# Optimization experiments

Hardware: AMD Instinct MI355X
Metric: run time of the kernel (lower is better)

## Reference

```python
import jax, jax.numpy as jnp
import numpy as np

# Static pyramid shapes (H, W) per level; must match setup_inputs().
SPATIAL_SHAPES = [(128, 128), (64, 64), (32, 32), (16, 16)]
N, LQ, D_MODEL, M, L, P = 2, 21760, 256, 8, 4, 4
D_HEAD = D_MODEL // M
LEN_IN = sum(h * w for h, w in SPATIAL_SHAPES)


def _bilinear_sample(v, grid, H, W):
    """torch.grid_sample(mode=bilinear, padding=zeros, align_corners=False).
    v: [B, H, W, D], grid: [B, Q, P, 2] (x, y) in [-1, 1] -> [B, Q, P, D]."""
    gx = (grid[..., 0] + 1.0) * (W * 0.5) - 0.5
    gy = (grid[..., 1] + 1.0) * (H * 0.5) - 0.5
    x0 = jnp.floor(gx)
    y0 = jnp.floor(gy)
    wx1 = gx - x0
    wy1 = gy - y0
    b = jnp.arange(v.shape[0])[:, None, None]

    def gather(yi, xi):
        valid = (xi >= 0) & (xi <= W - 1) & (yi >= 0) & (yi <= H - 1)
        xc = jnp.clip(xi, 0, W - 1).astype(jnp.int32)
        yc = jnp.clip(yi, 0, H - 1).astype(jnp.int32)
        return v[b, yc, xc] * valid[..., None].astype(v.dtype)

    return (gather(y0, x0) * ((1 - wy1) * (1 - wx1))[..., None]
            + gather(y0, x0 + 1) * ((1 - wy1) * wx1)[..., None]
            + gather(y0 + 1, x0) * (wy1 * (1 - wx1))[..., None]
            + gather(y0 + 1, x0 + 1) * (wy1 * wx1)[..., None])


def setup_inputs() -> dict:
    key = jax.random.key(0)
    ks = jax.random.split(key, 12)
    s = 0.02
    return {
        "query": jax.random.normal(ks[0], (N, LQ, D_MODEL), jnp.float32),
        "reference_points": jax.random.uniform(ks[1], (N, LQ, L, 2), jnp.float32),
        "value": jax.random.normal(ks[2], (N, LEN_IN, D_MODEL), jnp.float32),
        "value_spatial_shapes": jnp.array(SPATIAL_SHAPES, jnp.int32),
        "W_val": jax.random.normal(ks[3], (D_MODEL, D_MODEL), jnp.float32) * s,
        "b_val": jnp.zeros((D_MODEL,), jnp.float32),
        "W_off": jax.random.normal(ks[4], (D_MODEL, M * L * P * 2), jnp.float32) * s,
        "b_off": jax.random.normal(ks[5], (M * L * P * 2,), jnp.float32) * s,
        "W_attn": jax.random.normal(ks[6], (D_MODEL, M * L * P), jnp.float32) * s,
        "b_attn": jnp.zeros((M * L * P,), jnp.float32),
        "W_out": jax.random.normal(ks[7], (D_MODEL, D_MODEL), jnp.float32) * s,
        "b_out": jnp.zeros((D_MODEL,), jnp.float32),
    }


def reference(query, reference_points, value, value_spatial_shapes,
              W_val, b_val, W_off, b_off, W_attn, b_attn, W_out, b_out):
    # value_spatial_shapes is treated as static (SPATIAL_SHAPES) for jit safety.
    v = (value @ W_val + b_val).reshape(N, LEN_IN, M, D_HEAD)
    off = (query @ W_off + b_off).reshape(N, LQ, M, L, P, 2)
    aw = jax.nn.softmax((query @ W_attn + b_attn).reshape(N, LQ, M, L * P), axis=-1)
    aw = aw.reshape(N, LQ, M, L, P)
    # normalizer stacks (W, H) -> x normalized by W, y by H
    norm = jnp.array([[w, h] for h, w in SPATIAL_SHAPES], dtype=query.dtype)
    loc = reference_points[:, :, None, :, None, :] + off / norm[None, None, None, :, None, :]
    grid = 2.0 * loc - 1.0  # [N, LQ, M, L, P, 2]

    out = jnp.zeros((N * M, LQ, D_HEAD), query.dtype)
    start = 0
    for lid, (H, W) in enumerate(SPATIAL_SHAPES):
        vl = v[:, start:start + H * W].reshape(N, H, W, M, D_HEAD)
        vl = vl.transpose(0, 3, 1, 2, 4).reshape(N * M, H, W, D_HEAD)
        gl = grid[:, :, :, lid].transpose(0, 2, 1, 3, 4).reshape(N * M, LQ, P, 2)
        sl = _bilinear_sample(vl, gl, H, W)  # [N*M, LQ, P, D]
        wl = aw[:, :, :, lid].transpose(0, 2, 1, 3).reshape(N * M, LQ, P)
        out = out + jnp.einsum('bqpd,bqp->bqd', sl, wl)
        start += H * W

    out = out.reshape(N, M, LQ, D_HEAD).transpose(0, 2, 1, 3).reshape(N, LQ, D_MODEL)
    return out @ W_out + b_out
```

## Files before the change

### kernel.cpp

```cpp
#include <hip/hip_runtime.h>

typedef __attribute__((ext_vector_type(8))) short short8;
typedef __attribute__((ext_vector_type(4))) float floatx4;

#define N_    2
#define LQ_   21760
#define D_    256
#define M_    8
#define L_    4
#define P_    4
#define DH_   32
#define LEN_  21760
#define BQ    16

__constant__ int c_start[4] = {0, 16384, 20480, 21504};
__constant__ int c_HW[4]    = {128, 64, 32, 16};

#define WT_BYTE_OFF 22282240u

__device__ __forceinline__ unsigned short f2bf(float f) {
  unsigned int u = __builtin_bit_cast(unsigned int, f);
  u += 0x7fffu + ((u >> 16) & 1u);
  return (unsigned short)(u >> 16);
}
__device__ __forceinline__ float bf2f(unsigned short s) {
  return __builtin_bit_cast(float, ((unsigned int)s) << 16);
}
__device__ __forceinline__ float bflo(unsigned int u) {
  return __builtin_bit_cast(float, u << 16);
}
__device__ __forceinline__ float bfhi(unsigned int u) {
  return __builtin_bit_cast(float, u & 0xffff0000u);
}

__global__ __launch_bounds__(256) void prep_kernel(
    const float* __restrict__ Woff, const float* __restrict__ Watt,
    const float* __restrict__ Wout, const float* __restrict__ Wv,
    unsigned short* __restrict__ wt) {
  const int b = blockIdx.x, t = threadIdx.x;
  const float* src; int ncols, n; unsigned short* dst;
  if (b < 256)      { src = Woff; ncols = 256; n = b;       dst = wt + 0      + n * 256; }
  else if (b < 384) { src = Watt; ncols = 128; n = b - 256; dst = wt + 65536  + n * 256; }
  else if (b < 640) { src = Wout; ncols = 256; n = b - 384; dst = wt + 98304  + n * 256; }
  else              { src = Wv;   ncols = 256; n = b - 640; dst = wt + 163840 + n * 256; }
  dst[t] = f2bf(src[(size_t)t * ncols + n]);
}

__global__ __launch_bounds__(256, 2) void vproj_kernel(
    const float* __restrict__ value, const unsigned short* __restrict__ Wvt,
    const float* __restrict__ bv, unsigned short* __restrict__ vout) {
  __shared__ unsigned short vs[64][264];
  const int t = threadIdx.x;
  const int r0 = blockIdx.x * 64;
  {
    const int c2 = (t & 127) * 2;
    const int rb = t >> 7;
#pragma unroll
    for (int i = 0; i < 32; ++i) {
      int rr = rb + i * 2;
      float2 v = *(const float2*)(value + (size_t)(r0 + rr) * D_ + c2);
      *(unsigned int*)&vs[rr][c2] = (unsigned int)f2bf(v.x) | ((unsigned int)f2bf(v.y) << 16);
    }
  }
  __syncthreads();
  const int wave = t >> 6, lane = t & 63;
  const int arow = wave * 16 + (lane & 15);
  const int kg = (lane >> 4) * 8;
  floatx4 acc[16] = {};
  for (int kk = 0; kk < 8; ++kk) {
    const int k0 = kk * 32;
    short8 af = *(const short8*)&vs[arow][k0 + kg];
#pragma unroll
    for (int ct = 0; ct < 16; ++ct) {
      const int col = ct * 16 + (lane & 15);
      short8 bf = *(const short8*)(Wvt + col * 256 + k0 + kg);
      acc[ct] = __builtin_amdgcn_mfma_f32_16x16x32_bf16(af, bf, acc[ct], 0, 0, 0);
    }
  }
  const int n = (r0 >= LEN_) ? 1 : 0;
  const int pixbase = r0 - n * LEN_ + wave * 16 + ((lane >> 4) * 4);
#pragma unroll
  for (int ct = 0; ct < 16; ++ct) {
    const int gc = ct * 16 + (lane & 15);
    const int m = gc >> 5, d = gc & 31;
    const float bb = bv[gc];
    unsigned short* ob = vout + ((size_t)(n * M_ + m) * LEN_) * DH_ + d;
#pragma unroll
    for (int j = 0; j < 4; ++j)
      ob[(size_t)(pixbase + j) * DH_] = f2bf(acc[ct][j] + bb);
  }
}

__global__ __launch_bounds__(256, 5) void msda_kernel(
    const float* __restrict__ query, const float* __restrict__ refp,
    const unsigned short* __restrict__ wt,
    const float* __restrict__ boff, const float* __restrict__ batt,
    const float* __restrict__ bout,
    const unsigned short* __restrict__ vproj, float* __restrict__ out) {
  __shared__ unsigned short qs[BQ][264];
  __shared__ unsigned short offb[BQ][256];
  __shared__ float awb[BQ][128];
  __shared__ short idxs2[2][128];
  __shared__ float wls2[2][128][4];

  const int t = threadIdx.x;
  const int lb = (blockIdx.x & 7) * 340 + (blockIdx.x >> 3);
  const int qg0 = lb * BQ;
  const int n = qg0 / LQ_;

  {
    const int c2 = (t & 127) * 2;
    const int rb = t >> 7;
#pragma unroll
    for (int i = 0; i < 8; ++i) {
      int rr = rb + i * 2;
      float2 v = *(const float2*)(query + (size_t)(qg0 + rr) * D_ + c2);
      *(unsigned int*)&qs[rr][c2] = (unsigned int)f2bf(v.x) | ((unsigned int)f2bf(v.y) << 16);
    }
  }
  __syncthreads();

  const int wave = t >> 6, lane = t & 63;
  const int arow = lane & 15;
  const int kg = (lane >> 4) * 8;
  const int row0 = (lane >> 4) * 4;

  {
    floatx4 acc[6] = {};
    for (int kk = 0; kk < 8; ++kk) {
      const int k0 = kk * 32;
      short8 af = *(const short8*)&qs[arow][k0 + kg];
#pragma unroll
      for (int i = 0; i < 6; ++i) {
        const int col = wave * 96 + i * 16 + (lane & 15);
        const unsigned short* bp = (col < 256) ? (wt + col * 256)
                                               : (wt + 65536 + (col - 256) * 256);
        short8 bf = *(const short8*)(bp + k0 + kg);
        acc[i] = __builtin_amdgcn_mfma_f32_16x16x32_bf16(af, bf, acc[i], 0, 0, 0);
      }
    }
#pragma unroll
    for (int i = 0; i < 6; ++i) {
      const int col = wave * 96 + i * 16 + (lane & 15);
      if (col < 256) {
        const float bb = boff[col];
#pragma unroll
        for (int j = 0; j < 4; ++j) offb[row0 + j][col] = f2bf(acc[i][j] + bb);
      } else {
        const float bb = batt[col - 256];
#pragma unroll
        for (int j = 0; j < 4; ++j) awb[row0 + j][col - 256] = acc[i][j] + bb;
      }
    }
  }
  __syncthreads();

  if (t < 128) {
    const int q = t >> 3, m = t & 7;
    float v[16]; float mx = -1e30f;
#pragma unroll
    for (int s = 0; s < 16; ++s) { v[s] = awb[q][m * 16 + s]; mx = fmaxf(mx, v[s]); }
    float sum = 0.f;
#pragma unroll
    for (int s = 0; s < 16; ++s) { v[s] = __expf(v[s] - mx); sum += v[s]; }
    const float inv = 1.f / sum;
#pragma unroll
    for (int s = 0; s < 16; ++s) awb[q][m * 16 + s] = v[s] * inv;
  }
  __syncthreads();

  const int m_g = t >> 5;
  const int g = t & 31;
  const int sp   = g >> 4;
  const int rsel = (g >> 3) & 1;
  const int csel = (g >> 2) & 1;
  const int wsel = (g >> 2) & 3;
  const int doct = g & 3;
  const char* vbyte = (const char*)vproj + (size_t)(n * M_ + m_g) * LEN_ * DH_ * 2;

  for (int q = 0; q < BQ; ++q) {
    const int slot = q & 1;
    if (t < 128) {
      const int l = (t >> 2) & 3;
      const int Wl = c_HW[l];
      const int st = c_start[l];
      const float rx = refp[(((size_t)(qg0 + q)) * L_ + l) * 2 + 0];
      const float ry = refp[(((size_t)(qg0 + q)) * L_ + l) * 2 + 1];
      const float gx = rx * (float)Wl + bf2f(offb[q][2 * t])     - 0.5f;
      const float gy = ry * (float)Wl + bf2f(offb[q][2 * t + 1]) - 0.5f;
      const float fx0 = floorf(gx), fy0 = floorf(gy);
      const int x0 = (int)fx0, y0 = (int)fy0;
      const float wx1 = gx - fx0, wy1 = gy - fy0;
      const float wx0 = 1.f - wx1, wy0 = 1.f - wy1;
      const float a = awb[q][t];
      const bool vx0 = (x0 >= 0) && (x0 < Wl);
      const bool vx1 = (x0 + 1 >= 0) && (x0 + 1 < Wl);
      const bool vy0 = (y0 >= 0) && (y0 < Wl);
      const bool vy1 = (y0 + 1 >= 0) && (y0 + 1 < Wl);
      idxs2[slot][t] = (short)(st + y0 * Wl + x0);
      wls2[slot][t][0] = (vy0 && vx0) ? wy0 * wx0 * a : 0.f;
      wls2[slot][t][1] = (vy0 && vx1) ? wy0 * wx1 * a : 0.f;
      wls2[slot][t][2] = (vy1 && vx0) ? wy1 * wx0 * a : 0.f;
      wls2[slot][t][3] = (vy1 && vx1) ? wy1 * wx1 * a : 0.f;
    }
    __syncthreads();

    const int sidb = m_g * 16;
    uint4 u0, u1, u2, u3, u4, u5, u6, u7;
    float w0, w1, w2, w3, w4, w5, w6, w7;
#define GLD(i, WLC)                                                        \
    {                                                                      \
      const int s_ = 2 * (i) + sp;                                         \
      const int ix_ = (int)idxs2[slot][sidb + s_];                         \
      w##i = wls2[slot][sidb + s_][wsel];                                  \
      int ofs_ = (ix_ + rsel * (WLC) + csel) * 64 + doct * 16;             \
      ofs_ = (ofs_ > 0) ? ofs_ : 0;                                        \
      u##i = *(const uint4*)(vbyte + ofs_);                                \
    }
    GLD(0, 128) GLD(1, 128) GLD(2, 64) GLD(3, 64)
    GLD(4, 32)  GLD(5, 32)  GLD(6, 16) GLD(7, 16)
#undef GLD

    float acc0 = 0.f, acc1 = 0.f, acc2 = 0.f, acc3 = 0.f;
    float acc4 = 0.f, acc5 = 0.f, acc6 = 0.f, acc7 = 0.f;
#define FMA8(i)                                                            \
    acc0 += bflo(u##i.x) * w##i; acc1 += bfhi(u##i.x) * w##i;              \
    acc2 += bflo(u##i.y) * w##i; acc3 += bfhi(u##i.y) * w##i;              \
    acc4 += bflo(u##i.z) * w##i; acc5 += bfhi(u##i.z) * w##i;              \
    acc6 += bflo(u##i.w) * w##i; acc7 += bfhi(u##i.w) * w##i;
    FMA8(0) FMA8(1) FMA8(2) FMA8(3) FMA8(4) FMA8(5) FMA8(6) FMA8(7)
#undef FMA8

    acc0 += __shfl_xor(acc0, 4);  acc1 += __shfl_xor(acc1, 4);
    acc2 += __shfl_xor(acc2, 4);  acc3 += __shfl_xor(acc3, 4);
    acc4 += __shfl_xor(acc4, 4);  acc5 += __shfl_xor(acc5, 4);
    acc6 += __shfl_xor(acc6, 4);  acc7 += __shfl_xor(acc7, 4);
    acc0 += __shfl_xor(acc0, 8);  acc1 += __shfl_xor(acc1, 8);
    acc2 += __shfl_xor(acc2, 8);  acc3 += __shfl_xor(acc3, 8);
    acc4 += __shfl_xor(acc4, 8);  acc5 += __shfl_xor(acc5, 8);
    acc6 += __shfl_xor(acc6, 8);  acc7 += __shfl_xor(acc7, 8);
    acc0 += __shfl_xor(acc0, 16); acc1 += __shfl_xor(acc1, 16);
    acc2 += __shfl_xor(acc2, 16); acc3 += __shfl_xor(acc3, 16);
    acc4 += __shfl_xor(acc4, 16); acc5 += __shfl_xor(acc5, 16);
    acc6 += __shfl_xor(acc6, 16); acc7 += __shfl_xor(acc7, 16);

    if (g < 4) {
      uint4 st4;
      st4.x = (unsigned int)f2bf(acc0) | ((unsigned int)f2bf(acc1) << 16);
      st4.y = (unsigned int)f2bf(acc2) | ((unsigned int)f2bf(acc3) << 16);
      st4.z = (unsigned int)f2bf(acc4) | ((unsigned int)f2bf(acc5) << 16);
      st4.w = (unsigned int)f2bf(acc6) | ((unsigned int)f2bf(acc7) << 16);
      *(uint4*)&qs[q][m_g * 32 + doct * 8] = st4;
    }
  }
  __syncthreads();

  {
    floatx4 acc[4] = {};
    for (int kk = 0; kk < 8; ++kk) {
      const int k0 = kk * 32;
      short8 af = *(const short8*)&qs[arow][k0 + kg];
#pragma unroll
      for (int i = 0; i < 4; ++i) {
        const int col = wave * 64 + i * 16 + (lane & 15);
        short8 bf = *(const short8*)(wt + 98304 + col * 256 + k0 + kg);
        acc[i] = __builtin_amdgcn_mfma_f32_16x16x32_bf16(af, bf, acc[i], 0, 0, 0);
      }
    }
#pragma unroll
    for (int i = 0; i < 4; ++i) {
      const int col = wave * 64 + i * 16 + (lane & 15);
      const float bb = bout[col];
#pragma unroll
      for (int j = 0; j < 4; ++j)
        out[(size_t)(qg0 + row0 + j) * D_ + col] = acc[i][j] + bb;
    }
  }
}

extern "C" void kernel_launch(void* const* d_in, const int* in_sizes, int n_in,
                              void* d_out, int out_size, void* d_ws, size_t ws_size,
                              hipStream_t stream) {
  const float* query = (const float*)d_in[0];
  const float* refp  = (const float*)d_in[1];
  const float* value = (const float*)d_in[2];
  const float* Wv    = (const float*)d_in[4];
  const float* bv    = (const float*)d_in[5];
  const float* Woff  = (const float*)d_in[6];
  const float* boff  = (const float*)d_in[7];
  const float* Watt  = (const float*)d_in[8];
  const float* batt  = (const float*)d_in[9];
  const float* Wout  = (const float*)d_in[10];
  const float* bout  = (const float*)d_in[11];
  float* out = (float*)d_out;

  unsigned short* vproj = (unsigned short*)d_ws;
  unsigned short* wt    = (unsigned short*)((char*)d_ws + WT_BYTE_OFF);
  const unsigned short* Wvt = wt + 163840;

  dim3 blk(256);
  hipLaunchKernelGGL(prep_kernel, dim3(896), blk, 0, stream, Woff, Watt, Wout, Wv, wt);
  hipLaunchKernelGGL(vproj_kernel, dim3((N_ * LEN_) / 64), blk, 0, stream, value, Wvt, bv, vproj);
  hipLaunchKernelGGL(msda_kernel, dim3((N_ * LQ_) / BQ), blk, 0, stream,
                     query, refp, wt, boff, batt, bout, vproj, out);
}
```

Baseline: 239.6 us.

## Make sampling stage wave-local, removing per-query block barriers

Each wave now computes its own sampling indices and bilinear weights, for its two heads and two queries at a time, into wave-private shared slots. This removes the per-query __syncthreads and the 128-thread-only setup phase. Reference points are preloaded into registers up front, and a waves_per_eu hint is added. The risk is higher register pressure from the rp array and the unrolled two-query body. Correctness also depends on wave-level lockstep for the shared-memory handoff, since there is no explicit barrier.

```diff
diff --git a/kernel.cpp b/kernel.cpp
--- a/kernel.cpp
+++ b/kernel.cpp
@@ -91,7 +91,9 @@
   }
 }
 
-__global__ __launch_bounds__(256, 5) void msda_kernel(
+__global__ __launch_bounds__(256, 5)
+__attribute__((amdgpu_waves_per_eu(4, 5)))
+void msda_kernel(
     const float* __restrict__ query, const float* __restrict__ refp,
     const unsigned short* __restrict__ wt,
     const float* __restrict__ boff, const float* __restrict__ batt,
@@ -100,8 +102,8 @@
   __shared__ unsigned short qs[BQ][264];
   __shared__ unsigned short offb[BQ][256];
   __shared__ float awb[BQ][128];
-  __shared__ short idxs2[2][128];
-  __shared__ float wls2[2][128][4];
+  __shared__ short sidx[4][2][2][16];
+  __shared__ float swls[4][2][2][16][4];
 
   const int t = threadIdx.x;
   const int lb = (blockIdx.x & 7) * 340 + (blockIdx.x >> 3);
@@ -169,88 +171,96 @@
   }
   __syncthreads();
 
-  const int m_g = t >> 5;
-  const int g = t & 31;
-  const int sp   = g >> 4;
-  const int rsel = (g >> 3) & 1;
-  const int csel = (g >> 2) & 1;
-  const int wsel = (g >> 2) & 3;
-  const int doct = g & 3;
+  const int qo  = lane >> 5;
+  const int sh  = (lane >> 4) & 1;
+  const int ss  = lane & 15;
+  const int slv = ss >> 2;
+  const int WlS = 128 >> slv;
+  const int stS = c_start[slv];
+  const int st_eq = (2 * wave + sh) * 16 + ss;
+  const int hg = lane >> 5;
+  const int m_g = 2 * wave + hg;
+  const int g = lane & 31;
+  const int sp = g >> 4, rsel = (g >> 3) & 1, csel = (g >> 2) & 1;
+  const int wsel = (g >> 2) & 3, doct = g & 3;
   const char* vbyte = (const char*)vproj + (size_t)(n * M_ + m_g) * LEN_ * DH_ * 2;
 
-  for (int q = 0; q < BQ; ++q) {
-    const int slot = q & 1;
-    if (t < 128) {
-      const int l = (t >> 2) & 3;
-      const int Wl = c_HW[l];
-      const int st = c_start[l];
-      const float rx = refp[(((size_t)(qg0 + q)) * L_ + l) * 2 + 0];
-      const float ry = refp[(((size_t)(qg0 + q)) * L_ + l) * 2 + 1];
-      const float gx = rx * (float)Wl + bf2f(offb[q][2 * t])     - 0.5f;
-      const float gy = ry * (float)Wl + bf2f(offb[q][2 * t + 1]) - 0.5f;
+  const float2* refp2 = (const float2*)refp;
+  float2 rp[8];
+#pragma unroll
+  for (int e = 0; e < 8; ++e)
+    rp[e] = refp2[(size_t)(qg0 + 2 * e + qo) * 4 + slv];
+
+  for (int e = 0; e < 8; ++e) {
+    {
+      const int q = 2 * e + qo;
+      const float gx = rp[e].x * (float)WlS + bf2f(offb[q][2 * st_eq])     - 0.5f;
+      const float gy = rp[e].y * (float)WlS + bf2f(offb[q][2 * st_eq + 1]) - 0.5f;
       const float fx0 = floorf(gx), fy0 = floorf(gy);
       const int x0 = (int)fx0, y0 = (int)fy0;
       const float wx1 = gx - fx0, wy1 = gy - fy0;
       const float wx0 = 1.f - wx1, wy0 = 1.f - wy1;
-      const float a = awb[q][t];
-      const bool vx0 = (x0 >= 0) && (x0 < Wl);
-      const bool vx1 = (x0 + 1 >= 0) && (x0 + 1 < Wl);
-      const bool vy0 = (y0 >= 0) && (y0 < Wl);
-      const bool vy1 = (y0 + 1 >= 0) && (y0 + 1 < Wl);
-      idxs2[slot][t] = (short)(st + y0 * Wl + x0);
-      wls2[slot][t][0] = (vy0 && vx0) ? wy0 * wx0 * a : 0.f;
-      wls2[slot][t][1] = (vy0 && vx1) ? wy0 * wx1 * a : 0.f;
-      wls2[slot][t][2] = (vy1 && vx0) ? wy1 * wx0 * a : 0.f;
-      wls2[slot][t][3] = (vy1 && vx1) ? wy1 * wx1 * a : 0.f;
-    }
-    __syncthreads();
-
-    const int sidb = m_g * 16;
-    uint4 u0, u1, u2, u3, u4, u5, u6, u7;
-    float w0, w1, w2, w3, w4, w5, w6, w7;
+      const float a = awb[q][st_eq];
+      const bool vx0 = (x0 >= 0) && (x0 < WlS);
+      const bool vx1 = (x0 + 1 >= 0) && (x0 + 1 < WlS);
+      const bool vy0 = (y0 >= 0) && (y0 < WlS);
+      const bool vy1 = (y0 + 1 >= 0) && (y0 + 1 < WlS);
+      sidx[wave][qo][sh][ss] = (short)(stS + y0 * WlS + x0);
+      swls[wave][qo][sh][ss][0] = (vy0 && vx0) ? wy0 * wx0 * a : 0.f;
+      swls[wave][qo][sh][ss][1] = (vy0 && vx1) ? wy0 * wx1 * a : 0.f;
+      swls[wave][qo][sh][ss][2] = (vy1 && vx0) ? wy1 * wx0 * a : 0.f;
+      swls[wave][qo][sh][ss][3] = (vy1 && vx1) ? wy1 * wx1 * a : 0.f;
+    }
+
+#pragma unroll
+    for (int qo2 = 0; qo2 < 2; ++qo2) {
+      const int qp = 2 * e + qo2;
+      uint4 u0, u1, u2, u3, u4, u5, u6, u7;
+      float w0, w1, w2, w3, w4, w5, w6, w7;
 #define GLD(i, WLC)                                                        \
-    {                                                                      \
-      const int s_ = 2 * (i) + sp;                                         \
-      const int ix_ = (int)idxs2[slot][sidb + s_];                         \
-      w##i = wls2[slot][sidb + s_][wsel];                                  \
-      int ofs_ = (ix_ + rsel * (WLC) + csel) * 64 + doct * 16;             \
-      ofs_ = (ofs_ > 0) ? ofs_ : 0;                                        \
-      u##i = *(const uint4*)(vbyte + ofs_);                                \
-    }
-    GLD(0, 128) GLD(1, 128) GLD(2, 64) GLD(3, 64)
-    GLD(4, 32)  GLD(5, 32)  GLD(6, 16) GLD(7, 16)
+      {                                                                    \
+        const int s_ = 2 * (i) + sp;                                       \
+        const int ix_ = (int)sidx[wave][qo2][hg][s_];                      \
+        w##i = swls[wave][qo2][hg][s_][wsel];                              \
+        int ofs_ = (ix_ + rsel * (WLC) + csel) * 64 + doct * 16;           \
+        ofs_ = (ofs_ > 0) ? ofs_ : 0;                                      \
+        u##i = *(const uint4*)(vbyte + ofs_);                              \
+      }
+      GLD(0, 128) GLD(1, 128) GLD(2, 64) GLD(3, 64)
+      GLD(4, 32)  GLD(5, 32)  GLD(6, 16) GLD(7, 16)
 #undef GLD
 
-    float acc0 = 0.f, acc1 = 0.f, acc2 = 0.f, acc3 = 0.f;
-    float acc4 = 0.f, acc5 = 0.f, acc6 = 0.f, acc7 = 0.f;
+      float acc0 = 0.f, acc1 = 0.f, acc2 = 0.f, acc3 = 0.f;
+      float acc4 = 0.f, acc5 = 0.f, acc6 = 0.f, acc7 = 0.f;
 #define FMA8(i)                                                            \
-    acc0 += bflo(u##i.x) * w##i; acc1 += bfhi(u##i.x) * w##i;              \
-    acc2 += bflo(u##i.y) * w##i; acc3 += bfhi(u##i.y) * w##i;              \
-    acc4 += bflo(u##i.z) * w##i; acc5 += bfhi(u##i.z) * w##i;              \
-    acc6 += bflo(u##i.w) * w##i; acc7 += bfhi(u##i.w) * w##i;
-    FMA8(0) FMA8(1) FMA8(2) FMA8(3) FMA8(4) FMA8(5) FMA8(6) FMA8(7)
+      acc0 += bflo(u##i.x) * w##i; acc1 += bfhi(u##i.x) * w##i;            \
+      acc2 += bflo(u##i.y) * w##i; acc3 += bfhi(u##i.y) * w##i;            \
+      acc4 += bflo(u##i.z) * w##i; acc5 += bfhi(u##i.z) * w##i;            \
+      acc6 += bflo(u##i.w) * w##i; acc7 += bfhi(u##i.w) * w##i;
+      FMA8(0) FMA8(1) FMA8(2) FMA8(3) FMA8(4) FMA8(5) FMA8(6) FMA8(7)
 #undef FMA8
 
-    acc0 += __shfl_xor(acc0, 4);  acc1 += __shfl_xor(acc1, 4);
-    acc2 += __shfl_xor(acc2, 4);  acc3 += __shfl_xor(acc3, 4);
-    acc4 += __shfl_xor(acc4, 4);  acc5 += __shfl_xor(acc5, 4);
-    acc6 += __shfl_xor(acc6, 4);  acc7 += __shfl_xor(acc7, 4);
-    acc0 += __shfl_xor(acc0, 8);  acc1 += __shfl_xor(acc1, 8);
-    acc2 += __shfl_xor(acc2, 8);  acc3 += __shfl_xor(acc3, 8);
-    acc4 += __shfl_xor(acc4, 8);  acc5 += __shfl_xor(acc5, 8);
-    acc6 += __shfl_xor(acc6, 8);  acc7 += __shfl_xor(acc7, 8);
-    acc0 += __shfl_xor(acc0, 16); acc1 += __shfl_xor(acc1, 16);
-    acc2 += __shfl_xor(acc2, 16); acc3 += __shfl_xor(acc3, 16);
-    acc4 += __shfl_xor(acc4, 16); acc5 += __shfl_xor(acc5, 16);
-    acc6 += __shfl_xor(acc6, 16); acc7 += __shfl_xor(acc7, 16);
-
-    if (g < 4) {
-      uint4 st4;
-      st4.x = (unsigned int)f2bf(acc0) | ((unsigned int)f2bf(acc1) << 16);
-      st4.y = (unsigned int)f2bf(acc2) | ((unsigned int)f2bf(acc3) << 16);
-      st4.z = (unsigned int)f2bf(acc4) | ((unsigned int)f2bf(acc5) << 16);
-      st4.w = (unsigned int)f2bf(acc6) | ((unsigned int)f2bf(acc7) << 16);
-      *(uint4*)&qs[q][m_g * 32 + doct * 8] = st4;
+      acc0 += __shfl_xor(acc0, 4);  acc1 += __shfl_xor(acc1, 4);
+      acc2 += __shfl_xor(acc2, 4);  acc3 += __shfl_xor(acc3, 4);
+      acc4 += __shfl_xor(acc4, 4);  acc5 += __shfl_xor(acc5, 4);
+      acc6 += __shfl_xor(acc6, 4);  acc7 += __shfl_xor(acc7, 4);
+      acc0 += __shfl_xor(acc0, 8);  acc1 += __shfl_xor(acc1, 8);
+      acc2 += __shfl_xor(acc2, 8);  acc3 += __shfl_xor(acc3, 8);
+      acc4 += __shfl_xor(acc4, 8);  acc5 += __shfl_xor(acc5, 8);
+      acc6 += __shfl_xor(acc6, 8);  acc7 += __shfl_xor(acc7, 8);
+      acc0 += __shfl_xor(acc0, 16); acc1 += __shfl_xor(acc1, 16);
+      acc2 += __shfl_xor(acc2, 16); acc3 += __shfl_xor(acc3, 16);
+      acc4 += __shfl_xor(acc4, 16); acc5 += __shfl_xor(acc5, 16);
+      acc6 += __shfl_xor(acc6, 16); acc7 += __shfl_xor(acc7, 16);
+
+      if (g < 4) {
+        uint4 st4;
+        st4.x = (unsigned int)f2bf(acc0) | ((unsigned int)f2bf(acc1) << 16);
+        st4.y = (unsigned int)f2bf(acc2) | ((unsigned int)f2bf(acc3) << 16);
+        st4.z = (unsigned int)f2bf(acc4) | ((unsigned int)f2bf(acc5) << 16);
+        st4.w = (unsigned int)f2bf(acc6) | ((unsigned int)f2bf(acc7) << 16);
+        *(uint4*)&qs[qp][m_g * 32 + doct * 8] = st4;
+      }
     }
   }
   __syncthreads();
```

Result: faster. 232.6 us (-2.9%).
